# Optimization experiments

Hardware: AMD Instinct MI355X
Metric: run time of the kernel (lower is better)

Reference implementation:

```python
import jax, jax.numpy as jnp
from jax import lax
import numpy as np

B, L1, L2 = 64, 1024, 1024


def setup_inputs() -> dict:
    key = jax.random.key(0)
    ks = jax.random.split(key, 6)
    s1 = 1.0 / np.sqrt(L1)
    s2 = 1.0 / np.sqrt(L2)
    return {
        "a": jax.random.normal(ks[0], (B, L1), dtype=jnp.float32),
        "b": jax.random.normal(ks[1], (B, L2), dtype=jnp.float32),
        # nn.Linear(L1, L1) and nn.Linear(L2, L2) params (PyTorch default uniform init range)
        "W1": jax.random.uniform(ks[2], (L1, L1), jnp.float32, -s1, s1),
        "b1": jax.random.uniform(ks[3], (L1,), jnp.float32, -s1, s1),
        "W2": jax.random.uniform(ks[4], (L2, L2), jnp.float32, -s2, s2),
        "b2": jax.random.uniform(ks[5], (L2,), jnp.float32, -s2, s2),
    }


def _dtw_cost(cost):
    """DTW accumulated-cost DP for one [N, M] pairwise-cost matrix.

    R[i,j] = cost[i,j] + min(R[i-1,j-1], R[i-1,j], R[i,j-1]).
    The within-row dependency x[j] = c[j] + min(m[j], x[j-1]) is a min-plus
    prefix: x[j] = S[j] + cummin(m - S_{j-1}) with S = cumsum(c), which lets
    each row be computed in parallel (wavefront-equivalent vectorization).
    Returns the scalar DTW distance R[N-1, M-1].
    """
    dt = cost.dtype
    row0 = jnp.cumsum(cost[0])  # R[0, :]

    def step(prev_row, c_row):
        # m[j] = min(R[i-1, j], R[i-1, j-1]);  j=0 has no (i-1, j-1) neighbor
        shifted = jnp.concatenate([jnp.full((1,), jnp.inf, dt), prev_row[:-1]])
        m = jnp.minimum(prev_row, shifted)
        S = jnp.cumsum(c_row)
        S_prev = jnp.concatenate([jnp.zeros((1,), dt), S[:-1]])
        row = S + lax.associative_scan(jnp.minimum, m - S_prev)
        return row, None

    last_row, _ = lax.scan(step, row0, cost[1:])
    return last_row[-1]


def reference(a, b, W1, b1, W2, b2):
    # seq1 / seq2 linear projections over the time axis
    a_p = a @ W1.T + b1  # [B, L1]
    b_p = b @ W2.T + b2  # [B, L2]
    # squared-euclidean pairwise cost (scipy.sqeuclidean on scalar elements)
    cost = (a_p[:, :, None] - b_p[:, None, :]) ** 2  # [B, L1, L2]
    return jax.vmap(_dtw_cost)(cost)  # [B] DTW distances
```

## Files before the change

### kernel.cpp

```cpp
#include <hip/hip_runtime.h>
#include <math.h>


#define L 1024
#define BATCH 64

__global__ __launch_bounds__(256) void proj_kernel(
    const float* __restrict__ a, const float* __restrict__ b,
    const float* __restrict__ W1, const float* __restrict__ b1,
    const float* __restrict__ W2, const float* __restrict__ b2,
    float* __restrict__ ap, float* __restrict__ bp, int KC) {
  int part = blockIdx.x >> 7;
  int sub = blockIdx.x & 127;
  const float* X;
  const float* W;
  const float* bias;
  float* out;
  int i0;
  if (sub < 64) {
    X = a; W = W1; bias = b1; out = ap + part * BATCH * L; i0 = sub * 16;
  } else {
    X = b; W = W2; bias = b2; out = bp + part * BATCH * L; i0 = (sub - 64) * 16;
  }

  __shared__ float a_s[64][36];
  __shared__ float w_s[16][36];

  int tid = threadIdx.x;
  int lane_b = tid & 63;
  int iq = tid >> 6;

  float acc[4] = {0.f, 0.f, 0.f, 0.f};

  int kbeg = part * KC;
  int kend = kbeg + KC;
  for (int k0 = kbeg; k0 < kend; k0 += 32) {
    {
      int row = tid >> 2;
      int kl = (tid & 3) * 8;
      const float4* src = reinterpret_cast<const float4*>(&X[row * L + k0 + kl]);
      float4 v0 = src[0];
      float4 v1 = src[1];
      *reinterpret_cast<float4*>(&a_s[row][kl]) = v0;
      *reinterpret_cast<float4*>(&a_s[row][kl + 4]) = v1;
    }
    {
      int row = tid >> 4;
      int kl = (tid & 15) * 2;
      float2 v = *reinterpret_cast<const float2*>(&W[(i0 + row) * L + k0 + kl]);
      w_s[row][kl] = v.x;
      w_s[row][kl + 1] = v.y;
    }
    __syncthreads();
    #pragma unroll
    for (int kl = 0; kl < 32; kl += 4) {
      float4 av = *reinterpret_cast<const float4*>(&a_s[lane_b][kl]);
      #pragma unroll
      for (int m = 0; m < 4; ++m) {
        float4 wv = *reinterpret_cast<const float4*>(&w_s[iq * 4 + m][kl]);
        acc[m] += av.x * wv.x + av.y * wv.y + av.z * wv.z + av.w * wv.w;
      }
    }
    __syncthreads();
  }

  #pragma unroll
  for (int m = 0; m < 4; ++m) {
    int i = i0 + iq * 4 + m;
    float bv = (part == 0) ? bias[i] : 0.f;
    out[lane_b * L + i] = acc[m] + bv;
  }
}


#define NW 4
#define CPL 4
#define KBAR 32
#define OFF 95
#define DMAX (OFF * (NW - 1) + 63)
#define NG 43
#define NSTEPS (NG * KBAR)
#define APPAD (DMAX + NSTEPS + 64)

__device__ __forceinline__ float dpp_shr1_z(float v) {
  int r = __builtin_amdgcn_update_dpp(0, __float_as_int(v), 0x138, 0xf, 0xf,
                                      true);
  return __int_as_float(r);
}

__device__ __forceinline__ float dpp_shl1_z(float v) {
  int r = __builtin_amdgcn_update_dpp(0, __float_as_int(v), 0x130, 0xf, 0xf,
                                      true);
  return __int_as_float(r);
}

__device__ __forceinline__ float min3f(float x, float y, float z) {
  float r;
  asm("v_min3_f32 %0, %1, %2, %3" : "=v"(r) : "v"(x), "v"(y), "v"(z));
  return r;
}

__global__ __launch_bounds__(256, 1) void dtw_kernel(
    const float* __restrict__ app, const float* __restrict__ bpp,
    float* __restrict__ out, int parts) {
  const int b = blockIdx.x;
  const int tid = threadIdx.x;
  const int w = tid >> 6;
  const int t = tid & 63;
  const int woff = w * OFF;
  const int D = woff + t;
  const float INF = INFINITY;

  __shared__ float ap_pad[APPAD];
  __shared__ float ring[NW - 1][64];

  for (int idx = tid; idx < APPAD; idx += 256) {
    int src = idx - DMAX;
    float v = 0.f;
    if ((unsigned)src < (unsigned)L) {
      v = app[b * L + src];
      for (int p = 1; p < parts; ++p) v += app[p * BATCH * L + b * L + src];
    }
    ap_pad[idx] = v;
  }

  float4 bv = *reinterpret_cast<const float4*>(&bpp[b * L + tid * CPL]);
  for (int p = 1; p < parts; ++p) {
    float4 u = *reinterpret_cast<const float4*>(
        &bpp[p * BATCH * L + b * L + tid * CPL]);
    bv.x += u.x; bv.y += u.y; bv.z += u.z; bv.w += u.w;
  }
  const float bpv0 = bv.x, bpv1 = bv.y, bpv2 = bv.z, bpv3 = bv.w;

  float p0 = INF, p1 = INF, p2 = INF, p3 = INF;
  float right = INF, prev_left = INF;
  float vprod = INF;
  float ringchunk = INF;
  float apv = 0.f;
  float apchunk = 0.f;
  const bool lane0 = (t == 0);
  const bool lane63 = (t == 63);
  const int ap_base = DMAX - woff + t;

  __syncthreads();

#define DTW_GROUP(s0v, PRED, FIRSTG)                                         \
  {                                                                          \
    const int s0 = (s0v);                                                    \
    apchunk = ap_pad[ap_base + s0];                                          \
    if (w == 0)                                                              \
      ringchunk = ((FIRSTG) && lane0) ? 0.f : INF;                           \
    else if (t < KBAR)                                                       \
      ringchunk = ring[w - 1][(s0 - woff + t) & 63];                         \
    _Pragma("unroll")                                                        \
    for (int k = 0; k < KBAR; ++k) {                                         \
      float shifted = dpp_shr1_z(right);                                     \
      float left = lane0 ? ringchunk : shifted;                              \
      ringchunk = dpp_shl1_z(ringchunk);                                     \
      float apsh = dpp_shr1_z(apv);                                          \
      apv = lane0 ? apchunk : apsh;                                          \
      apchunk = dpp_shl1_z(apchunk);                                         \
      int ii = s0 + k - D;                                                   \
      if (!(PRED) || ((unsigned)ii < (unsigned)L)) {                         \
        float dprev = prev_left;                                             \
        if ((FIRSTG) && k == 1 && w == 0 && t == 0) dprev = INF;             \
        prev_left = left;                                                    \
        float d0 = apv - bpv0, d1 = apv - bpv1;                              \
        float d2 = apv - bpv2, d3 = apv - bpv3;                              \
        float x = left, bb;                                                  \
        bb = min3f(p0, dprev, x); x = __builtin_fmaf(d0, d0, bb);            \
        dprev = p0; p0 = x;                                                  \
        bb = min3f(p1, dprev, x); x = __builtin_fmaf(d1, d1, bb);            \
        dprev = p1; p1 = x;                                                  \
        bb = min3f(p2, dprev, x); x = __builtin_fmaf(d2, d2, bb);            \
        dprev = p2; p2 = x;                                                  \
        bb = min3f(p3, dprev, x); x = __builtin_fmaf(d3, d3, bb);            \
        p3 = x;                                                              \
        right = x;                                                           \
      }                                                                      \
      vprod = dpp_shl1_z(vprod);                                             \
      vprod = lane63 ? right : vprod;                                        \
    }                                                                        \
    if (w < NW - 1 && t >= 64 - KBAR)                                        \
      ring[w][(s0 + t - woff - (63 + KBAR)) & 63] = vprod;                   \
    __syncthreads();                                                         \
  }

  for (int g = 0; g < 11; ++g) DTW_GROUP(g * KBAR, true, g == 0);
  for (int g = 11; g < 32; ++g) DTW_GROUP(g * KBAR, false, false);
  for (int g = 32; g < NG; ++g) DTW_GROUP(g * KBAR, true, false);
#undef DTW_GROUP

  if (tid == NW * 64 - 1) out[b] = right;
}

extern "C" void kernel_launch(void* const* d_in, const int* in_sizes, int n_in,
                              void* d_out, int out_size, void* d_ws, size_t ws_size,
                              hipStream_t stream) {
  const float* a  = (const float*)d_in[0];
  const float* b  = (const float*)d_in[1];
  const float* W1 = (const float*)d_in[2];
  const float* b1 = (const float*)d_in[3];
  const float* W2 = (const float*)d_in[4];
  const float* b2 = (const float*)d_in[5];
  float* out = (float*)d_out;

  size_t per_part = (size_t)2 * BATCH * L * sizeof(float);
  int parts = 1;
  if (ws_size >= 4 * per_part) parts = 4;
  else if (ws_size >= 2 * per_part) parts = 2;

  float* ap = (float*)d_ws;
  float* bp = ap + (size_t)parts * BATCH * L;

  proj_kernel<<<128 * parts, 256, 0, stream>>>(a, b, W1, b1, W2, b2,
                                               ap, bp, L / parts);
  dtw_kernel<<<BATCH, 256, 0, stream>>>(ap, bp, out, parts);
}
```

Baseline: 101.3 us.

## Skew DTW wavefront within each lane so the four columns update independently

Changes the DTW anti-diagonal schedule so each lane's four columns sit on successive diagonals. The four min3+fma updates per step no longer form a serial chain within a lane, and INF padding in the shared-memory copy of a replaces the per-step bounds predicate. The cost is a longer schedule (67 groups instead of 43) with smaller inter-wave offsets, plus more live registers for the two-row history and the shifted a values.

```diff
diff --git a/kernel.cpp b/kernel.cpp
--- a/kernel.cpp
+++ b/kernel.cpp
@@ -76,11 +76,10 @@
 #define NW 4
 #define CPL 4
 #define KBAR 32
-#define OFF 95
-#define DMAX (OFF * (NW - 1) + 63)
-#define NG 43
-#define NSTEPS (NG * KBAR)
-#define APPAD (DMAX + NSTEPS + 64)
+#define OFF 31
+#define NG 67
+#define APOFF 864
+#define APPAD 3048
 
 __device__ __forceinline__ float dpp_shr1_z(float v) {
   int r = __builtin_amdgcn_update_dpp(0, __float_as_int(v), 0x138, 0xf, 0xf,
@@ -107,91 +106,91 @@
   const int tid = threadIdx.x;
   const int w = tid >> 6;
   const int t = tid & 63;
-  const int woff = w * OFF;
-  const int D = woff + t;
+  const int woff = OFF * w;
   const float INF = INFINITY;
 
   __shared__ float ap_pad[APPAD];
   __shared__ float ring[NW - 1][64];
 
   for (int idx = tid; idx < APPAD; idx += 256) {
-    int src = idx - DMAX;
-    float v = 0.f;
+    int src = idx - APOFF;
+    float v = INF;
     if ((unsigned)src < (unsigned)L) {
       v = app[b * L + src];
       for (int p = 1; p < parts; ++p) v += app[p * BATCH * L + b * L + src];
     }
     ap_pad[idx] = v;
   }
-
-  float4 bv = *reinterpret_cast<const float4*>(&bpp[b * L + tid * CPL]);
+  if (tid < (NW - 1) * 64) reinterpret_cast<float*>(ring)[tid] = INF;
+
+  const int colb = tid * CPL;
+  float4 bv = *reinterpret_cast<const float4*>(&bpp[b * L + colb]);
   for (int p = 1; p < parts; ++p) {
     float4 u = *reinterpret_cast<const float4*>(
-        &bpp[p * BATCH * L + b * L + tid * CPL]);
+        &bpp[p * BATCH * L + b * L + colb]);
     bv.x += u.x; bv.y += u.y; bv.z += u.z; bv.w += u.w;
   }
   const float bpv0 = bv.x, bpv1 = bv.y, bpv2 = bv.z, bpv3 = bv.w;
 
-  float p0 = INF, p1 = INF, p2 = INF, p3 = INF;
-  float right = INF, prev_left = INF;
-  float vprod = INF;
-  float ringchunk = INF;
-  float apv = 0.f;
-  float apchunk = 0.f;
+  float p1_0 = INF, p1_1 = INF, p1_2 = INF, p1_3 = INF;
+  float p2_0 = INF, p2_1 = INF, p2_2 = INF, p2_3 = INF;
+  float A0 = INF, A1 = INF, A2 = INF, A3 = INF;
+  float ringchunk = INF, feedprev = INF, vprod = INF, apchunk;
+  float res = 0.f;
   const bool lane0 = (t == 0);
   const bool lane63 = (t == 63);
-  const int ap_base = DMAX - woff + t;
+  const int apbase = APOFF + t - (256 + OFF) * w;
 
   __syncthreads();
 
-#define DTW_GROUP(s0v, PRED, FIRSTG)                                         \
+#define DTW_GROUP(s0v, FIRSTG, LASTG)                                        \
   {                                                                          \
     const int s0 = (s0v);                                                    \
-    apchunk = ap_pad[ap_base + s0];                                          \
+    apchunk = ap_pad[apbase + s0];                                           \
     if (w == 0)                                                              \
-      ringchunk = ((FIRSTG) && lane0) ? 0.f : INF;                           \
+      ringchunk = INF;                                                       \
     else if (t < KBAR)                                                       \
-      ringchunk = ring[w - 1][(s0 - woff + t) & 63];                         \
+      ringchunk = ring[w - 1][(s0 + t - woff - 1) & 63];                     \
     _Pragma("unroll")                                                        \
     for (int k = 0; k < KBAR; ++k) {                                         \
-      float shifted = dpp_shr1_z(right);                                     \
-      float left = lane0 ? ringchunk : shifted;                              \
+      float sh1 = dpp_shr1_z(p1_3);                                          \
+      float sh2 = dpp_shr1_z(p2_3);                                          \
+      float sha = dpp_shr1_z(A3);                                            \
+      float p1m1 = lane0 ? ringchunk : sh1;                                  \
+      float p2m1 = lane0 ? feedprev : sh2;                                   \
+      if ((FIRSTG) && k == 0 && w == 0) p2m1 = lane0 ? 0.f : sh2;            \
+      feedprev = ringchunk;                                                  \
       ringchunk = dpp_shl1_z(ringchunk);                                     \
-      float apsh = dpp_shr1_z(apv);                                          \
-      apv = lane0 ? apchunk : apsh;                                          \
+      A3 = A2; A2 = A1; A1 = A0;                                             \
+      A0 = lane0 ? apchunk : sha;                                            \
       apchunk = dpp_shl1_z(apchunk);                                         \
-      int ii = s0 + k - D;                                                   \
-      if (!(PRED) || ((unsigned)ii < (unsigned)L)) {                         \
-        float dprev = prev_left;                                             \
-        if ((FIRSTG) && k == 1 && w == 0 && t == 0) dprev = INF;             \
-        prev_left = left;                                                    \
-        float d0 = apv - bpv0, d1 = apv - bpv1;                              \
-        float d2 = apv - bpv2, d3 = apv - bpv3;                              \
-        float x = left, bb;                                                  \
-        bb = min3f(p0, dprev, x); x = __builtin_fmaf(d0, d0, bb);            \
-        dprev = p0; p0 = x;                                                  \
-        bb = min3f(p1, dprev, x); x = __builtin_fmaf(d1, d1, bb);            \
-        dprev = p1; p1 = x;                                                  \
-        bb = min3f(p2, dprev, x); x = __builtin_fmaf(d2, d2, bb);            \
-        dprev = p2; p2 = x;                                                  \
-        bb = min3f(p3, dprev, x); x = __builtin_fmaf(d3, d3, bb);            \
-        p3 = x;                                                              \
-        right = x;                                                           \
-      }                                                                      \
+      float d0 = A0 - bpv0, d1 = A1 - bpv1;                                  \
+      float d2 = A2 - bpv2, d3 = A3 - bpv3;                                  \
+      float b0 = min3f(p1_0, p1m1, p2m1);                                    \
+      float b1 = min3f(p1_1, p1_0, p2_0);                                    \
+      float b2 = min3f(p1_2, p1_1, p2_1);                                    \
+      float b3 = min3f(p1_3, p1_2, p2_2);                                    \
+      float x0 = __builtin_fmaf(d0, d0, b0);                                 \
+      float x1 = __builtin_fmaf(d1, d1, b1);                                 \
+      float x2 = __builtin_fmaf(d2, d2, b2);                                 \
+      float x3 = __builtin_fmaf(d3, d3, b3);                                 \
+      p2_0 = p1_0; p2_1 = p1_1; p2_2 = p1_2; p2_3 = p1_3;                    \
+      p1_0 = x0; p1_1 = x1; p1_2 = x2; p1_3 = x3;                            \
       vprod = dpp_shl1_z(vprod);                                             \
-      vprod = lane63 ? right : vprod;                                        \
+      vprod = lane63 ? x3 : vprod;                                           \
+      if ((LASTG) && k == 27) res = x3;                                      \
     }                                                                        \
     if (w < NW - 1 && t >= 64 - KBAR)                                        \
-      ring[w][(s0 + t - woff - (63 + KBAR)) & 63] = vprod;                   \
+      ring[w][(s0 + t - 32 - woff) & 63] = vprod;                            \
     __syncthreads();                                                         \
   }
 
-  for (int g = 0; g < 11; ++g) DTW_GROUP(g * KBAR, true, g == 0);
-  for (int g = 11; g < 32; ++g) DTW_GROUP(g * KBAR, false, false);
-  for (int g = 32; g < NG; ++g) DTW_GROUP(g * KBAR, true, false);
+  DTW_GROUP(0, true, false);
+  for (int g = 1; g < NG - 1; ++g) DTW_GROUP(g * KBAR, false, false);
+  DTW_GROUP((NG - 1) * KBAR, false, true);
 #undef DTW_GROUP
 
-  if (tid == NW * 64 - 1) out[b] = right;
+  if (w == NW - 1 && t == 63) out[b] = res;
 }
 
 extern "C" void kernel_launch(void* const* d_in, const int* in_sizes, int n_in,
```

Result: slower. 106.1 us (+4.7%).
